# Performance work log

Hardware: AMD Instinct MI355X
Metric: run time of the kernel (lower is better)

Reference implementation:

```python
import jax, jax.numpy as jnp
import numpy as np

B, C, T, H, W = 4, 64, 8, 128, 128
DG = 8  # deformable groups; offset has 3*DG channels (dt, dh, dw per group, kernel 1x1x1)


def setup_inputs() -> dict:
    key = jax.random.key(0)
    k1, k2 = jax.random.split(key)
    x = jax.random.normal(k1, (B, C, T, H, W), dtype=jnp.float32)
    offset = jax.random.normal(k2, (B, 3 * DG, T, H, W), dtype=jnp.float32) * 2.0
    # frozen identity 1x1x1 conv weight and zero bias, as in the torch module
    weight = jnp.eye(C, dtype=jnp.float32).reshape(C, C, 1, 1, 1)
    bias = jnp.zeros((C,), dtype=jnp.float32)
    return {"x": x, "offset": offset, "weight": weight, "bias": bias}


def _deform_sample(x, offset):
    # x: [B, C, T, H, W]; offset: [B, 3*DG, T, H, W]
    Bs, Cs, Ts, Hs, Ws = x.shape
    Cg = Cs // DG
    off = offset.reshape(Bs, DG, 3, Ts, Hs, Ws)
    # absolute sampling coordinates per (batch, group, t, h, w)
    gt = jnp.arange(Ts, dtype=x.dtype)[:, None, None] + off[:, :, 0]
    gh = jnp.arange(Hs, dtype=x.dtype)[None, :, None] + off[:, :, 1]
    gw = jnp.arange(Ws, dtype=x.dtype)[None, None, :] + off[:, :, 2]
    t0 = jnp.floor(gt)
    h0 = jnp.floor(gh)
    w0 = jnp.floor(gw)
    N = Ts * Hs * Ws
    x_flat = x.reshape(Bs, DG, Cg, N)
    acc = jnp.zeros((Bs, DG, Cg, N), dtype=x.dtype)
    # trilinear interpolation over the 8 integer corners, zero outside bounds
    for ti, wt in ((t0, 1.0 - (gt - t0)), (t0 + 1.0, gt - t0)):
        for hi, wh in ((h0, 1.0 - (gh - h0)), (h0 + 1.0, gh - h0)):
            for wi, ww in ((w0, 1.0 - (gw - w0)), (w0 + 1.0, gw - w0)):
                valid = ((ti >= 0) & (ti < Ts) & (hi >= 0) & (hi < Hs)
                         & (wi >= 0) & (wi < Ws)).astype(x.dtype)
                tc = jnp.clip(ti, 0, Ts - 1).astype(jnp.int32)
                hc = jnp.clip(hi, 0, Hs - 1).astype(jnp.int32)
                wc = jnp.clip(wi, 0, Ws - 1).astype(jnp.int32)
                idx = ((tc * Hs + hc) * Ws + wc).reshape(Bs, DG, 1, N)
                vals = jnp.take_along_axis(
                    x_flat, jnp.broadcast_to(idx, (Bs, DG, Cg, N)), axis=3)
                wgt = (wt * wh * ww * valid).reshape(Bs, DG, 1, N)
                acc = acc + vals * wgt
    return acc.reshape(Bs, Cs, Ts, Hs, Ws)


def reference(x, offset, weight, bias):
    sampled = _deform_sample(x, offset)
    # 1x1x1 grouped(=1) conv accumulation with the (identity) weight
    out = jnp.einsum('oc,bcthw->bothw', weight[:, :, 0, 0, 0], sampled)
    return out + bias[None, :, None, None, None]
```

## Files before the change

### kernel.cpp

```cpp
#include <hip/hip_runtime.h>


#define Bc 4
#define Cc 64
#define Tc 8
#define Hc 128
#define Wc 128
#define DGc 8
#define Cgc (Cc / DGc)
#define Nc (Tc * Hc * Wc)
#define SITES (Bc * DGc * Nc)
#define XT_H_BYTES ((size_t)SITES * 16)

#define NXCD 8


__global__ __launch_bounds__(256) void transpose_kernel(
    const float* __restrict__ x, ushort* __restrict__ xt)
{
    __shared__ float lds[8][512];

    const int bid = blockIdx.x;
    const int bg  = bid >> 8;
    const int t   = (bid >> 5) & 7;
    const int h0  = (bid & 31) << 2;
    const int tid = threadIdx.x;

    const int nbase = (t << 14) | (h0 << 7);

#pragma unroll
    for (int q = 0; q < 4; ++q) {
        const int idx = q * 256 + tid;
        const int c   = idx >> 7;
        const int r   = idx & 127;
        const int hl  = r >> 5;
        const int wq  = (r & 31) << 2;
        const float* xp = x + (size_t)(bg * Cgc + c) * Nc + nbase + (hl << 7) + wq;
        float4 v;
        v.x = __builtin_nontemporal_load(xp + 0);
        v.y = __builtin_nontemporal_load(xp + 1);
        v.z = __builtin_nontemporal_load(xp + 2);
        v.w = __builtin_nontemporal_load(xp + 3);
        *(float4*)&lds[c][(hl << 7) + wq] = v;
    }
    __syncthreads();

#pragma unroll
    for (int q = 0; q < 2; ++q) {
        const int s = q * 256 + tid;
        union { float4 v; _Float16 h[8]; } pk;
#pragma unroll
        for (int c = 0; c < 8; ++c) pk.h[c] = (_Float16)lds[c][s];
        ((float4*)xt)[(size_t)bg * Nc + nbase + s] = pk.v;
    }
}

__global__ __launch_bounds__(256) void sample_kernel(
    const ushort* __restrict__ xt,
    const float* __restrict__ off,
    const float* __restrict__ bias,
    float* __restrict__ out)
{
    const int nb  = SITES / 256;
    const int bid = blockIdx.x;
    const int swz = (bid & (NXCD - 1)) * (nb / NXCD) + (bid >> 3);

    const int site = swz * 256 + threadIdx.x;
    const int n  = site & (Nc - 1);
    const int bg = site >> 17;
    const int g  = bg & (DGc - 1);
    const int b  = bg >> 3;

    const int w = n & (Wc - 1);
    const int h = (n >> 7) & (Hc - 1);
    const int t = n >> 14;

    const float* offp = off + ((size_t)b * (3 * DGc) + g * 3) * Nc + n;
    const float gt = (float)t + __builtin_nontemporal_load(offp + 0 * (size_t)Nc);
    const float gh = (float)h + __builtin_nontemporal_load(offp + 1 * (size_t)Nc);
    const float gw = (float)w + __builtin_nontemporal_load(offp + 2 * (size_t)Nc);

    const float t0f = floorf(gt), h0f = floorf(gh), w0f = floorf(gw);
    const float ft = gt - t0f, fh = gh - h0f, fw = gw - w0f;

    const int t0 = (int)t0f, h0i = (int)h0f, w0i = (int)w0f;
    const int tc0 = min(max(t0, 0), Tc - 1);
    const int tc1 = min(max(t0 + 1, 0), Tc - 1);
    const int hc0 = min(max(h0i, 0), Hc - 1);
    const int hc1 = min(max(h0i + 1, 0), Hc - 1);
    const int wlo = min(max(w0i, 0), Wc - 1);
    const int whi = min(max(w0i + 1, 0), Wc - 1);

    const float vt0 = (t0f >= 0.f  && t0f < (float)Tc)       ? (1.f - ft) : 0.f;
    const float vt1 = (t0f >= -1.f && t0f < (float)(Tc - 1)) ? ft         : 0.f;
    const float vh0 = (h0f >= 0.f  && h0f < (float)Hc)       ? (1.f - fh) : 0.f;
    const float vh1 = (h0f >= -1.f && h0f < (float)(Hc - 1)) ? fh         : 0.f;
    const float vw0 = (w0f >= 0.f  && w0f < (float)Wc)       ? (1.f - fw) : 0.f;
    const float vw1 = (w0f >= -1.f && w0f < (float)(Wc - 1)) ? fw         : 0.f;

    const int   tcs[2] = {tc0, tc1};
    const float vts[2] = {vt0, vt1};
    const int   hcs[2] = {hc0, hc1};
    const float vhs[2] = {vh0, vh1};

    const float4* __restrict__ xt4 = (const float4*)xt;
    const size_t base = (size_t)bg * Nc;

    float acc[8] = {0.f, 0.f, 0.f, 0.f, 0.f, 0.f, 0.f, 0.f};

#pragma unroll
    for (int i = 0; i < 2; ++i) {
#pragma unroll
        for (int j = 0; j < 2; ++j) {
            const float cw = vts[i] * vhs[j];
            const size_t rb = base + (size_t)(tcs[i] * (Hc * Wc) + hcs[j] * Wc);
            union { float4 v; _Float16 hx[8]; } lo, hi;
            lo.v = xt4[rb + wlo];
            hi.v = xt4[rb + whi];
            const float cl = cw * vw0;
            const float ch = cw * vw1;
#pragma unroll
            for (int k = 0; k < 8; ++k)
                acc[k] += cl * (float)lo.hx[k] + ch * (float)hi.hx[k];
        }
    }

    const int c0 = g * Cgc;
    float* ob = out + ((size_t)(b * Cc + c0)) * Nc + n;
#pragma unroll
    for (int k = 0; k < 8; ++k)
        __builtin_nontemporal_store(acc[k] + bias[c0 + k], ob + (size_t)k * Nc);
}

__global__ __launch_bounds__(256) void deform_sample_fallback(
    const float* __restrict__ x, const float* __restrict__ off,
    const float* __restrict__ bias, float* __restrict__ out)
{
    const int tid = blockIdx.x * blockDim.x + threadIdx.x;
    if (tid >= SITES) return;
    const int n  = tid & (Nc - 1);
    const int bg = tid >> 17;
    const int g  = bg & (DGc - 1);
    const int b  = bg >> 3;
    const int w = n & (Wc - 1);
    const int h = (n >> 7) & (Hc - 1);
    const int t = n >> 14;

    const float* offp = off + ((size_t)b * (3 * DGc) + g * 3) * Nc + n;
    const float gt = (float)t + offp[0 * Nc];
    const float gh = (float)h + offp[1 * Nc];
    const float gw = (float)w + offp[2 * Nc];
    const float t0 = floorf(gt), h0 = floorf(gh), w0 = floorf(gw);
    const float ft = gt - t0, fh = gh - h0, fw = gw - w0;

    int cidx[8]; float cwgt[8];
#pragma unroll
    for (int k = 0; k < 8; ++k) {
        const int it = k >> 2, ih = (k >> 1) & 1, iw = k & 1;
        const float tf = t0 + it, hf = h0 + ih, wf = w0 + iw;
        const bool valid = (tf >= 0.f) && (tf < (float)Tc) && (hf >= 0.f) &&
                           (hf < (float)Hc) && (wf >= 0.f) && (wf < (float)Wc);
        const float wt = it ? ft : (1.f - ft);
        const float wh = ih ? fh : (1.f - fh);
        const float ww = iw ? fw : (1.f - fw);
        int tc = (int)tf; tc = tc < 0 ? 0 : (tc > Tc - 1 ? Tc - 1 : tc);
        int hc = (int)hf; hc = hc < 0 ? 0 : (hc > Hc - 1 ? Hc - 1 : hc);
        int wc = (int)wf; wc = wc < 0 ? 0 : (wc > Wc - 1 ? Wc - 1 : wc);
        cidx[k] = (tc * Hc + hc) * Wc + wc;
        cwgt[k] = valid ? (wt * wh * ww) : 0.f;
    }
    const int c0 = g * Cgc;
    const float* xb = x + ((size_t)(b * Cc + c0)) * Nc;
    float* ob = out + ((size_t)(b * Cc + c0)) * Nc + n;
#pragma unroll
    for (int c = 0; c < Cgc; ++c) {
        const float* xc = xb + (size_t)c * Nc;
        float acc = 0.f;
#pragma unroll
        for (int k = 0; k < 8; ++k) acc += cwgt[k] * xc[cidx[k]];
        ob[(size_t)c * Nc] = acc + bias[c0 + c];
    }
}

extern "C" void kernel_launch(void* const* d_in, const int* in_sizes, int n_in,
                              void* d_out, int out_size, void* d_ws, size_t ws_size,
                              hipStream_t stream) {
    const float* x    = (const float*)d_in[0];
    const float* off  = (const float*)d_in[1];
    const float* bias = (const float*)d_in[3];
    float* out = (float*)d_out;

    if (ws_size >= XT_H_BYTES) {
        ushort* xt = (ushort*)d_ws;
        transpose_kernel<<<8192, 256, 0, stream>>>(x, xt);
        sample_kernel<<<SITES / 256, 256, 0, stream>>>(xt, off, bias, out);
    } else {
        deform_sample_fallback<<<SITES / 256, 256, 0, stream>>>(x, off, bias, out);
    }
}
```

Before: 345.8 us.

## Fuse transpose and sampling into one kernel with per-group atomic barrier

Replaces the separate transpose and sample kernels with one fused kernel. Each block converts a chunk of its (batch, group) slab into the packed fp16 channel-interleaved layout, then waits on a per-group atomic counter before sampling from that slab. Blocks are mapped so that each group's blocks share an XCD, aiming to keep the packed slab in local L2 and to save a launch. The cost is an extra memset launch and a spin barrier that relies on all 64 blocks of a group being resident together. A timeout path falls back to sampling directly from fp32 x if that assumption fails.

```diff
diff --git a/kernel.cpp b/kernel.cpp
--- a/kernel.cpp
+++ b/kernel.cpp
@@ -11,125 +11,143 @@
 #define Nc (Tc * Hc * Wc)
 #define SITES (Bc * DGc * Nc)
 #define XT_H_BYTES ((size_t)SITES * 16)
-
-#define NXCD 8
-
-
-__global__ __launch_bounds__(256) void transpose_kernel(
-    const float* __restrict__ x, ushort* __restrict__ xt)
-{
-    __shared__ float lds[8][512];
-
-    const int bid = blockIdx.x;
-    const int bg  = bid >> 8;
-    const int t   = (bid >> 5) & 7;
-    const int h0  = (bid & 31) << 2;
-    const int tid = threadIdx.x;
-
-    const int nbase = (t << 14) | (h0 << 7);
-
-#pragma unroll
-    for (int q = 0; q < 4; ++q) {
-        const int idx = q * 256 + tid;
-        const int c   = idx >> 7;
-        const int r   = idx & 127;
-        const int hl  = r >> 5;
-        const int wq  = (r & 31) << 2;
-        const float* xp = x + (size_t)(bg * Cgc + c) * Nc + nbase + (hl << 7) + wq;
-        float4 v;
-        v.x = __builtin_nontemporal_load(xp + 0);
-        v.y = __builtin_nontemporal_load(xp + 1);
-        v.z = __builtin_nontemporal_load(xp + 2);
-        v.w = __builtin_nontemporal_load(xp + 3);
-        *(float4*)&lds[c][(hl << 7) + wq] = v;
-    }
-    __syncthreads();
-
-#pragma unroll
-    for (int q = 0; q < 2; ++q) {
-        const int s = q * 256 + tid;
-        union { float4 v; _Float16 h[8]; } pk;
-#pragma unroll
-        for (int c = 0; c < 8; ++c) pk.h[c] = (_Float16)lds[c][s];
-        ((float4*)xt)[(size_t)bg * Nc + nbase + s] = pk.v;
-    }
-}
-
-__global__ __launch_bounds__(256) void sample_kernel(
-    const ushort* __restrict__ xt,
+#define WS_NEED (XT_H_BYTES + 128)
+
+#define GROUPS 32
+#define BPG 64
+#define GRID (GROUPS * BPG)
+
+__global__ __launch_bounds__(256, 8) void fused_kernel(
+    const float* __restrict__ x,
     const float* __restrict__ off,
     const float* __restrict__ bias,
-    float* __restrict__ out)
+    float* __restrict__ out,
+    ushort* __restrict__ xt,
+    unsigned* __restrict__ cnt)
 {
-    const int nb  = SITES / 256;
-    const int bid = blockIdx.x;
-    const int swz = (bid & (NXCD - 1)) * (nb / NXCD) + (bid >> 3);
-
-    const int site = swz * 256 + threadIdx.x;
-    const int n  = site & (Nc - 1);
-    const int bg = site >> 17;
-    const int g  = bg & (DGc - 1);
-    const int b  = bg >> 3;
-
-    const int w = n & (Wc - 1);
-    const int h = (n >> 7) & (Hc - 1);
-    const int t = n >> 14;
-
-    const float* offp = off + ((size_t)b * (3 * DGc) + g * 3) * Nc + n;
-    const float gt = (float)t + __builtin_nontemporal_load(offp + 0 * (size_t)Nc);
-    const float gh = (float)h + __builtin_nontemporal_load(offp + 1 * (size_t)Nc);
-    const float gw = (float)w + __builtin_nontemporal_load(offp + 2 * (size_t)Nc);
-
-    const float t0f = floorf(gt), h0f = floorf(gh), w0f = floorf(gw);
-    const float ft = gt - t0f, fh = gh - h0f, fw = gw - w0f;
-
-    const int t0 = (int)t0f, h0i = (int)h0f, w0i = (int)w0f;
-    const int tc0 = min(max(t0, 0), Tc - 1);
-    const int tc1 = min(max(t0 + 1, 0), Tc - 1);
-    const int hc0 = min(max(h0i, 0), Hc - 1);
-    const int hc1 = min(max(h0i + 1, 0), Hc - 1);
-    const int wlo = min(max(w0i, 0), Wc - 1);
-    const int whi = min(max(w0i + 1, 0), Wc - 1);
-
-    const float vt0 = (t0f >= 0.f  && t0f < (float)Tc)       ? (1.f - ft) : 0.f;
-    const float vt1 = (t0f >= -1.f && t0f < (float)(Tc - 1)) ? ft         : 0.f;
-    const float vh0 = (h0f >= 0.f  && h0f < (float)Hc)       ? (1.f - fh) : 0.f;
-    const float vh1 = (h0f >= -1.f && h0f < (float)(Hc - 1)) ? fh         : 0.f;
-    const float vw0 = (w0f >= 0.f  && w0f < (float)Wc)       ? (1.f - fw) : 0.f;
-    const float vw1 = (w0f >= -1.f && w0f < (float)(Wc - 1)) ? fw         : 0.f;
-
-    const int   tcs[2] = {tc0, tc1};
-    const float vts[2] = {vt0, vt1};
-    const int   hcs[2] = {hc0, hc1};
-    const float vhs[2] = {vh0, vh1};
+    const int bid  = blockIdx.x;
+    const int tid  = threadIdx.x;
+    const int xcd  = bid & 7;
+    const int j    = (bid >> 3) & 63;
+    const int grp  = xcd * 4 + ((bid >> 3) >> 6);
+    const int g    = grp & (DGc - 1);
+    const int b    = grp >> 3;
+
+    const size_t slab_f4 = (size_t)grp * Nc;
+    const float* xbase   = x + (size_t)grp * Cgc * Nc;
+    float4* xt4w = (float4*)xt;
+
+#pragma unroll
+    for (int q = 0; q < 8; ++q) {
+        const int s = j * 2048 + q * 256 + tid;
+        union { float4 v; _Float16 hx[8]; } pk;
+#pragma unroll
+        for (int c = 0; c < 8; ++c)
+            pk.hx[c] = (_Float16)__builtin_nontemporal_load(
+                           xbase + (size_t)c * Nc + s);
+        xt4w[slab_f4 + s] = pk.v;
+    }
+
+    __shared__ int okflag;
+    __syncthreads();
+    if (tid == 0) {
+        __threadfence();
+        __hip_atomic_fetch_add(&cnt[grp], 1u, __ATOMIC_RELEASE,
+                               __HIP_MEMORY_SCOPE_AGENT);
+        int ok = 1;
+        unsigned spins = 0;
+        while (__hip_atomic_load(&cnt[grp], __ATOMIC_ACQUIRE,
+                                 __HIP_MEMORY_SCOPE_AGENT) < (unsigned)BPG) {
+            __builtin_amdgcn_s_sleep(2);
+            if (++spins > 1000000u) { ok = 0; break; }
+        }
+        okflag = ok;
+        __threadfence();
+    }
+    __syncthreads();
+    const int ok = okflag;
 
     const float4* __restrict__ xt4 = (const float4*)xt;
-    const size_t base = (size_t)bg * Nc;
-
-    float acc[8] = {0.f, 0.f, 0.f, 0.f, 0.f, 0.f, 0.f, 0.f};
-
-#pragma unroll
-    for (int i = 0; i < 2; ++i) {
-#pragma unroll
-        for (int j = 0; j < 2; ++j) {
-            const float cw = vts[i] * vhs[j];
-            const size_t rb = base + (size_t)(tcs[i] * (Hc * Wc) + hcs[j] * Wc);
-            union { float4 v; _Float16 hx[8]; } lo, hi;
-            lo.v = xt4[rb + wlo];
-            hi.v = xt4[rb + whi];
-            const float cl = cw * vw0;
-            const float ch = cw * vw1;
-#pragma unroll
-            for (int k = 0; k < 8; ++k)
-                acc[k] += cl * (float)lo.hx[k] + ch * (float)hi.hx[k];
+    const float*  offp0 = off + ((size_t)b * (3 * DGc) + g * 3) * Nc;
+    const int     c0    = g * Cgc;
+    float* outb = out + (size_t)(b * Cc + c0) * Nc;
+
+    for (int q = 0; q < 8; ++q) {
+        const int n = j * 2048 + q * 256 + tid;
+        const int w = n & (Wc - 1);
+        const int h = (n >> 7) & (Hc - 1);
+        const int t = n >> 14;
+
+        const float gt = (float)t + __builtin_nontemporal_load(offp0 + 0 * (size_t)Nc + n);
+        const float gh = (float)h + __builtin_nontemporal_load(offp0 + 1 * (size_t)Nc + n);
+        const float gw = (float)w + __builtin_nontemporal_load(offp0 + 2 * (size_t)Nc + n);
+
+        const float t0f = floorf(gt), h0f = floorf(gh), w0f = floorf(gw);
+        const float ft = gt - t0f, fh = gh - h0f, fw = gw - w0f;
+
+        const int t0 = (int)t0f, h0i = (int)h0f, w0i = (int)w0f;
+        const int tc0 = min(max(t0, 0), Tc - 1);
+        const int tc1 = min(max(t0 + 1, 0), Tc - 1);
+        const int hc0 = min(max(h0i, 0), Hc - 1);
+        const int hc1 = min(max(h0i + 1, 0), Hc - 1);
+        const int wlo = min(max(w0i, 0), Wc - 1);
+        const int whi = min(max(w0i + 1, 0), Wc - 1);
+
+        const float vt0 = (t0f >= 0.f  && t0f < (float)Tc)       ? (1.f - ft) : 0.f;
+        const float vt1 = (t0f >= -1.f && t0f < (float)(Tc - 1)) ? ft         : 0.f;
+        const float vh0 = (h0f >= 0.f  && h0f < (float)Hc)       ? (1.f - fh) : 0.f;
+        const float vh1 = (h0f >= -1.f && h0f < (float)(Hc - 1)) ? fh         : 0.f;
+        const float vw0 = (w0f >= 0.f  && w0f < (float)Wc)       ? (1.f - fw) : 0.f;
+        const float vw1 = (w0f >= -1.f && w0f < (float)(Wc - 1)) ? fw         : 0.f;
+
+        const int   tcs[2] = {tc0, tc1};
+        const float vts[2] = {vt0, vt1};
+        const int   hcs[2] = {hc0, hc1};
+        const float vhs[2] = {vh0, vh1};
+
+        float acc[8] = {0.f, 0.f, 0.f, 0.f, 0.f, 0.f, 0.f, 0.f};
+
+        if (ok) {
+#pragma unroll
+            for (int i = 0; i < 2; ++i) {
+#pragma unroll
+                for (int jj = 0; jj < 2; ++jj) {
+                    const float cw = vts[i] * vhs[jj];
+                    const size_t rb = slab_f4
+                        + (size_t)(tcs[i] * (Hc * Wc) + hcs[jj] * Wc);
+                    union { float4 v; _Float16 hx[8]; } lo, hi;
+                    lo.v = xt4[rb + wlo];
+                    hi.v = xt4[rb + whi];
+                    const float cl = cw * vw0;
+                    const float ch = cw * vw1;
+#pragma unroll
+                    for (int k = 0; k < 8; ++k)
+                        acc[k] += cl * (float)lo.hx[k] + ch * (float)hi.hx[k];
+                }
+            }
+        } else {
+#pragma unroll
+            for (int i = 0; i < 2; ++i) {
+#pragma unroll
+                for (int jj = 0; jj < 2; ++jj) {
+                    const float cw = vts[i] * vhs[jj];
+                    const size_t rb = (size_t)(tcs[i] * (Hc * Wc) + hcs[jj] * Wc);
+                    const float cl = cw * vw0;
+                    const float ch = cw * vw1;
+#pragma unroll
+                    for (int k = 0; k < 8; ++k) {
+                        const float* xc = xbase + (size_t)k * Nc + rb;
+                        acc[k] += cl * xc[wlo] + ch * xc[whi];
+                    }
+                }
+            }
         }
-    }
-
-    const int c0 = g * Cgc;
-    float* ob = out + ((size_t)(b * Cc + c0)) * Nc + n;
-#pragma unroll
-    for (int k = 0; k < 8; ++k)
-        __builtin_nontemporal_store(acc[k] + bias[c0 + k], ob + (size_t)k * Nc);
+
+#pragma unroll
+        for (int k = 0; k < 8; ++k)
+            __builtin_nontemporal_store(acc[k] + bias[c0 + k],
+                                        outb + (size_t)k * Nc + n);
+    }
 }
 
 __global__ __launch_bounds__(256) void deform_sample_fallback(
@@ -190,10 +208,11 @@
     const float* bias = (const float*)d_in[3];
     float* out = (float*)d_out;
 
-    if (ws_size >= XT_H_BYTES) {
+    if (ws_size >= WS_NEED) {
         ushort* xt = (ushort*)d_ws;
-        transpose_kernel<<<8192, 256, 0, stream>>>(x, xt);
-        sample_kernel<<<SITES / 256, 256, 0, stream>>>(xt, off, bias, out);
+        unsigned* cnt = (unsigned*)((char*)d_ws + XT_H_BYTES);
+        hipMemsetAsync(cnt, 0, GROUPS * sizeof(unsigned), stream);
+        fused_kernel<<<GRID, 256, 0, stream>>>(x, off, bias, out, xt, cnt);
     } else {
         deform_sample_fallback<<<SITES / 256, 256, 0, stream>>>(x, off, bias, out);
     }
```

Result: slower. 842.3 us (+143.6%).
